# Kernel optimization log

Hardware: AMD Instinct MI355X
Metric: run time of the kernel (lower is better)

Reference implementation:

```python
import jax, jax.numpy as jnp
import numpy as np

N, E = 100000, 400000
IN, HID, H, D = 165, 128, 8, 16  # per-head dim D = HID // H
NUM_CLASSES = 2


def layer_norm(x, g, b, eps=1e-5):
    m = jnp.mean(x, axis=-1, keepdims=True)
    v = jnp.var(x, axis=-1, keepdims=True)
    return (x - m) / jnp.sqrt(v + eps) * g + b


def transformer_conv(x, src, dst, Wq, bq, Wk, bk, Wv, bv, Ws, bs):
    # x: [N, HID]; src/dst: [E]
    n = x.shape[0]
    q = (x @ Wq + bq).reshape(n, H, D)
    k = (x @ Wk + bk).reshape(n, H, D)
    v = (x @ Wv + bv).reshape(n, H, D)
    # per-edge attention logits: [E, H]
    alpha = jnp.sum(q[dst] * k[src], axis=-1) / jnp.sqrt(jnp.float32(D))
    # segment softmax over incoming edges of each destination node
    amax = jax.ops.segment_max(alpha, dst, num_segments=n)          # [N, H]
    amax = jnp.where(jnp.isfinite(amax), amax, 0.0)
    ex = jnp.exp(alpha - amax[dst])                                  # [E, H]
    denom = jax.ops.segment_sum(ex, dst, num_segments=n)            # [N, H]
    a = ex / (denom[dst] + 1e-16)
    msg = v[src] * a[..., None]                                      # [E, H, D]
    out = jax.ops.segment_sum(msg, dst, num_segments=n)             # [N, H, D]
    out = out.reshape(n, H * D)
    # root skip connection (root_weight=True, beta=False in PyG defaults)
    return out + x @ Ws + bs


def setup_inputs() -> dict:
    key = jax.random.key(0)
    ks = jax.random.split(key, 24)
    rn = lambda k, s: (jax.random.normal(k, s, jnp.float32) * 0.05)
    inp = {
        "x": jax.random.normal(ks[0], (N, IN), jnp.float32),
        "edge_index": jax.random.randint(ks[1], (2, E), 0, N, jnp.int32),
        "W_in": rn(ks[2], (IN, HID)), "b_in": jnp.zeros((HID,), jnp.float32),
        # layer 1 TransformerConv
        "Wq1": rn(ks[3], (HID, HID)), "bq1": jnp.zeros((HID,), jnp.float32),
        "Wk1": rn(ks[4], (HID, HID)), "bk1": jnp.zeros((HID,), jnp.float32),
        "Wv1": rn(ks[5], (HID, HID)), "bv1": jnp.zeros((HID,), jnp.float32),
        "Ws1": rn(ks[6], (HID, HID)), "bs1": jnp.zeros((HID,), jnp.float32),
        "g1": jnp.ones((HID,), jnp.float32), "be1": jnp.zeros((HID,), jnp.float32),
        # layer 2 TransformerConv
        "Wq2": rn(ks[7], (HID, HID)), "bq2": jnp.zeros((HID,), jnp.float32),
        "Wk2": rn(ks[8], (HID, HID)), "bk2": jnp.zeros((HID,), jnp.float32),
        "Wv2": rn(ks[9], (HID, HID)), "bv2": jnp.zeros((HID,), jnp.float32),
        "Ws2": rn(ks[10], (HID, HID)), "bs2": jnp.zeros((HID,), jnp.float32),
        "g2": jnp.ones((HID,), jnp.float32), "be2": jnp.zeros((HID,), jnp.float32),
        # classifier MLP
        "Wc1": rn(ks[11], (HID, HID // 2)), "bc1": jnp.zeros((HID // 2,), jnp.float32),
        "Wc2": rn(ks[12], (HID // 2, NUM_CLASSES)), "bc2": jnp.zeros((NUM_CLASSES,), jnp.float32),
    }
    return inp


def reference(x, edge_index, W_in, b_in,
              Wq1, bq1, Wk1, bk1, Wv1, bv1, Ws1, bs1, g1, be1,
              Wq2, bq2, Wk2, bk2, Wv2, bv2, Ws2, bs2, g2, be2,
              Wc1, bc1, Wc2, bc2):
    src, dst = edge_index[0], edge_index[1]
    h = x @ W_in + b_in                                   # input projection
    h_new = transformer_conv(h, src, dst, Wq1, bq1, Wk1, bk1, Wv1, bv1, Ws1, bs1)
    h = layer_norm(h + h_new, g1, be1)                    # dropout = identity (eval)
    h_new = transformer_conv(h, src, dst, Wq2, bq2, Wk2, bk2, Wv2, bv2, Ws2, bs2)
    h = layer_norm(h + h_new, g2, be2)
    return jax.nn.relu(h @ Wc1 + bc1) @ Wc2 + bc2         # [N, num_classes]
```

## Files before the change

kernel.cpp:

```cpp
#include <hip/hip_runtime.h>
#include <hip/hip_bf16.h>

#define NN 100000
#define EE 400000
#define IN_DIM 165
#define KPAD 192
#define HID 128
#define C1 64
#define NC 2
#define SCANB 256
#define NBLK 391
#define NBD2 782

typedef const float* fpp;
typedef __hip_bfloat16 bf16;
typedef __attribute__((ext_vector_type(8))) short s16x8;
typedef __attribute__((ext_vector_type(4))) float f32x4;

__device__ __forceinline__ float bflo(unsigned u) { return __uint_as_float(u << 16); }
__device__ __forceinline__ float bfhi(unsigned u) { return __uint_as_float(u & 0xFFFF0000u); }
__device__ __forceinline__ unsigned short bfbits(float f) {
    bf16 h = __float2bfloat16(f);
    return *reinterpret_cast<unsigned short*>(&h);
}

__global__ void k_cvt_weights(fpp W_in, fpp Wq1, fpp Wk1, fpp Wv1, fpp Ws1,
                              fpp Wq2, fpp Wk2, fpp Wv2, fpp Ws2, fpp Wc1,
                              unsigned short* __restrict__ winpack,
                              unsigned short* __restrict__ wpack,
                              unsigned short* __restrict__ wc1t) {
    int idx = blockIdx.x * blockDim.x + threadIdx.x;
    if (idx < 24576) {
        int n = idx / KPAD, k = idx % KPAD;
        float v = (k < IN_DIM) ? W_in[k * HID + n] : 0.f;
        winpack[idx] = bfbits(v);
    } else if (idx < 155648) {
        int local = idx - 24576;
        int j = local >> 14;
        int l14 = local & 16383;
        int n = l14 >> 7, k = l14 & 127;
        const float* src;
        switch (j) {
            case 0: src = Wq1; break; case 1: src = Wk1; break;
            case 2: src = Wv1; break; case 3: src = Ws1; break;
            case 4: src = Wq2; break; case 5: src = Wk2; break;
            case 6: src = Wv2; break; default: src = Ws2; break;
        }
        wpack[local] = bfbits(src[k * HID + n]);
    } else {
        int local = idx - 155648;
        int n = local >> 7, k = local & 127;
        wc1t[local] = bfbits(Wc1[k * C1 + n]);
    }
}

__global__ void k_cvt_x(fpp x, unsigned short* __restrict__ xb) {
    int i = blockIdx.x * blockDim.x + threadIdx.x;
    int row = i / 24, c = i % 24;
    s16x8 us;
#pragma unroll
    for (int j = 0; j < 8; j++) {
        int col = c * 8 + j;
        float v = (col < IN_DIM) ? x[(size_t)row * IN_DIM + col] : 0.f;
        us[j] = (short)bfbits(v);
    }
    *(s16x8*)(xb + (size_t)row * KPAD + c * 8) = us;
}

__global__ void k_hist(const int* __restrict__ dst, int* __restrict__ deg) {
    int e = blockIdx.x * blockDim.x + threadIdx.x;
    if (e < EE) atomicAdd(&deg[dst[e]], 1);
}
__global__ void k_scan1(const int* __restrict__ deg, int* __restrict__ pos,
                        int* __restrict__ bsum, int n) {
    __shared__ int tmp[SCANB];
    int t = threadIdx.x, i = blockIdx.x * SCANB + t;
    int v = (i < n) ? deg[i] : 0;
    tmp[t] = v; __syncthreads();
    for (int off = 1; off < SCANB; off <<= 1) {
        int x = (t >= off) ? tmp[t - off] : 0;
        __syncthreads();
        tmp[t] += x;
        __syncthreads();
    }
    if (i < n) pos[i] = tmp[t] - v;
    if (t == SCANB - 1) bsum[blockIdx.x] = tmp[t];
}
__global__ void k_scan2(int* __restrict__ bsum, int nb) {
    __shared__ int tmp[512];
    int t = threadIdx.x;
    int v = (t < nb) ? bsum[t] : 0;
    tmp[t] = v; __syncthreads();
    for (int off = 1; off < 512; off <<= 1) {
        int x = (t >= off) ? tmp[t - off] : 0;
        __syncthreads();
        tmp[t] += x;
        __syncthreads();
    }
    if (t < nb) bsum[t] = tmp[t] - v;
}
__global__ void k_scan3(int* __restrict__ pos, const int* __restrict__ bsum, int n) {
    int i = blockIdx.x * blockDim.x + threadIdx.x;
    if (i < n) pos[i] += bsum[blockIdx.x];
}
__global__ void k_fill(const int* __restrict__ src, const int* __restrict__ dst,
                       int* __restrict__ pos, int* __restrict__ esrc) {
    int e = blockIdx.x * blockDim.x + threadIdx.x;
    if (e < EE) {
        int p = atomicAdd(&pos[dst[e]], 1);
        esrc[p] = src[e];
    }
}
__global__ void k_pack_csr(const int* __restrict__ pos, const int* __restrict__ deg,
                           int2* __restrict__ csr2) {
    int i = blockIdx.x * blockDim.x + threadIdx.x;
    if (i < NN) {
        int c = deg[i];
        csr2[i] = make_int2(pos[i] - c, c);
    }
}

__global__ __launch_bounds__(256) void k_dense_in(const unsigned short* __restrict__ xb,
                                                  const unsigned short* __restrict__ winpack,
                                                  fpp b_in, unsigned short* __restrict__ hb) {
    __shared__ unsigned short smem[18432];
    unsigned short* As = smem;
    unsigned short* Ws = smem + 9216;
    int row0 = blockIdx.x * 128;
    int t = threadIdx.x, lane = t & 63, w = t >> 6;
    int quad = lane >> 4, l16 = lane & 15;
    int m_off = (w >> 1) * 64, n_off = (w & 1) * 64;

    f32x4 acc[4][4];
    float bias_v[4];
#pragma unroll
    for (int ni = 0; ni < 4; ni++) bias_v[ni] = b_in[n_off + ni * 16 + l16];
#pragma unroll
    for (int mi = 0; mi < 4; mi++)
#pragma unroll
        for (int ni = 0; ni < 4; ni++)
            acc[mi][ni] = (f32x4){bias_v[ni], bias_v[ni], bias_v[ni], bias_v[ni]};

    for (int kc = 0; kc < 3; kc++) {
        __syncthreads();
        for (int i = 0; i < 4; i++) {
            int g = t + i * 256;
            int r = g >> 3, c = g & 7;
            int rg = min(row0 + r, NN - 1);
            *(s16x8*)(As + r * 72 + c * 8) =
                *(const s16x8*)(xb + (size_t)rg * KPAD + kc * 64 + c * 8);
            *(s16x8*)(Ws + r * 72 + c * 8) =
                *(const s16x8*)(winpack + r * KPAD + kc * 64 + c * 8);
        }
        __syncthreads();
#pragma unroll
        for (int ks = 0; ks < 2; ks++) {
            int k0 = ks * 32;
            s16x8 a[4], b[4];
#pragma unroll
            for (int mi = 0; mi < 4; mi++)
                a[mi] = *(const s16x8*)(As + (m_off + mi * 16 + l16) * 72 + k0 + quad * 8);
#pragma unroll
            for (int ni = 0; ni < 4; ni++)
                b[ni] = *(const s16x8*)(Ws + (n_off + ni * 16 + l16) * 72 + k0 + quad * 8);
#pragma unroll
            for (int mi = 0; mi < 4; mi++)
#pragma unroll
                for (int ni = 0; ni < 4; ni++)
                    acc[mi][ni] = __builtin_amdgcn_mfma_f32_16x16x32_bf16(
                        a[mi], b[ni], acc[mi][ni], 0, 0, 0);
        }
    }
    __syncthreads();
    unsigned short* Cs = smem;
#pragma unroll
    for (int mi = 0; mi < 4; mi++)
#pragma unroll
        for (int ni = 0; ni < 4; ni++)
#pragma unroll
            for (int r = 0; r < 4; r++)
                Cs[(m_off + mi * 16 + quad * 4 + r) * 136 + n_off + ni * 16 + l16] =
                    bfbits(acc[mi][ni][r]);
    __syncthreads();
    for (int i = 0; i < 8; i++) {
        int g = t + i * 256;
        int r = g >> 4, c = g & 15;
        if (row0 + r < NN)
            *(s16x8*)(hb + (size_t)(row0 + r) * HID + c * 8) =
                *(const s16x8*)(Cs + r * 136 + c * 8);
    }
}

__global__ __launch_bounds__(256) void k_dense4(const unsigned short* __restrict__ hb,
                                                const unsigned short* __restrict__ wpackL,
                                                fpp bq, fpp bk, fpp bv, fpp bs,
                                                bf16* __restrict__ qb, bf16* __restrict__ kb,
                                                bf16* __restrict__ vb, bf16* __restrict__ agg) {
    __shared__ unsigned short As[128 * 136];
    __shared__ unsigned short Ws[128 * 136];
    int row0 = blockIdx.x * 128;
    int t = threadIdx.x, lane = t & 63, w = t >> 6;
    int quad = lane >> 4, l16 = lane & 15;
    int m_off = (w >> 1) * 64, n_off = (w & 1) * 64;

    for (int i = 0; i < 8; i++) {
        int g = t + i * 256;
        int r = g >> 4, c = g & 15;
        int rg = min(row0 + r, NN - 1);
        *(s16x8*)(As + r * 136 + c * 8) = *(const s16x8*)(hb + (size_t)rg * HID + c * 8);
    }
    __syncthreads();

    s16x8 afr[4][4];
#pragma unroll
    for (int ks = 0; ks < 4; ks++)
#pragma unroll
        for (int mi = 0; mi < 4; mi++)
            afr[ks][mi] = *(const s16x8*)(As + (m_off + mi * 16 + l16) * 136 + ks * 32 + quad * 8);

    for (int nc = 0; nc < 4; nc++) {
        const float* bp; bf16* tp;
        if (nc == 0)      { bp = bq; tp = qb; }
        else if (nc == 1) { bp = bk; tp = kb; }
        else if (nc == 2) { bp = bv; tp = vb; }
        else              { bp = bs; tp = agg; }

        __syncthreads();
        for (int i = 0; i < 8; i++) {
            int g = t + i * 256;
            int r = g >> 4, c = g & 15;
            *(s16x8*)(Ws + r * 136 + c * 8) =
                *(const s16x8*)(wpackL + nc * 16384 + r * HID + c * 8);
        }
        __syncthreads();

        f32x4 acc[4][4];
        float bias_v[4];
#pragma unroll
        for (int ni = 0; ni < 4; ni++) bias_v[ni] = bp[n_off + ni * 16 + l16];
#pragma unroll
        for (int mi = 0; mi < 4; mi++)
#pragma unroll
            for (int ni = 0; ni < 4; ni++)
                acc[mi][ni] = (f32x4){bias_v[ni], bias_v[ni], bias_v[ni], bias_v[ni]};

#pragma unroll
        for (int ks = 0; ks < 4; ks++) {
            s16x8 b[4];
#pragma unroll
            for (int ni = 0; ni < 4; ni++)
                b[ni] = *(const s16x8*)(Ws + (n_off + ni * 16 + l16) * 136 + ks * 32 + quad * 8);
#pragma unroll
            for (int mi = 0; mi < 4; mi++)
#pragma unroll
                for (int ni = 0; ni < 4; ni++)
                    acc[mi][ni] = __builtin_amdgcn_mfma_f32_16x16x32_bf16(
                        afr[ks][mi], b[ni], acc[mi][ni], 0, 0, 0);
        }
        __syncthreads();

        unsigned short* Cs = Ws;
#pragma unroll
        for (int mi = 0; mi < 4; mi++)
#pragma unroll
            for (int ni = 0; ni < 4; ni++)
#pragma unroll
                for (int r = 0; r < 4; r++)
                    Cs[(m_off + mi * 16 + quad * 4 + r) * 136 + n_off + ni * 16 + l16] =
                        bfbits(acc[mi][ni][r]);
        __syncthreads();
        for (int i = 0; i < 8; i++) {
            int g = t + i * 256;
            int r = g >> 4, c = g & 15;
            if (row0 + r < NN)
                *(s16x8*)((unsigned short*)tp + (size_t)(row0 + r) * HID + c * 8) =
                    *(const s16x8*)(Cs + r * 136 + c * 8);
        }
    }
}

__global__ void k_agg_ln(const bf16* __restrict__ qb, const bf16* __restrict__ kb,
                         const bf16* __restrict__ vb, const int2* __restrict__ csr2,
                         const int* __restrict__ esrc, const bf16* __restrict__ agg,
                         unsigned short* __restrict__ hb, fpp g, fpp b) {
    int wid = (blockIdx.x * blockDim.x + threadIdx.x) >> 6;
    if (wid >= NN) return;
    int lane = threadIdx.x & 63;
    int d = wid;
    unsigned qu = ((const unsigned*)(qb + (size_t)d * HID))[lane];
    float q0 = bflo(qu) * 0.25f, q1 = bfhi(qu) * 0.25f;
    int2 se = csr2[d];
    int start = se.x, cnt = se.y;
    float m = -INFINITY, L = 0.f, o0 = 0.f, o1 = 0.f;
    for (int base = 0; base < cnt; base += 64) {
        int nc = min(64, cnt - base);
        int sj = (lane < nc) ? esrc[start + base + lane] : 0;
        int j = 0;
        for (; j + 1 < nc; j += 2) {
            int s0 = __shfl(sj, j, 64);
            int s1 = __shfl(sj, j + 1, 64);
            unsigned ku0 = ((const unsigned*)(kb + (size_t)s0 * HID))[lane];
            unsigned ku1 = ((const unsigned*)(kb + (size_t)s1 * HID))[lane];
            unsigned vu0 = ((const unsigned*)(vb + (size_t)s0 * HID))[lane];
            unsigned vu1 = ((const unsigned*)(vb + (size_t)s1 * HID))[lane];
            float t0 = q0 * bflo(ku0) + q1 * bfhi(ku0);
            float t1 = q0 * bflo(ku1) + q1 * bfhi(ku1);
            t0 += __shfl_xor(t0, 1, 64); t1 += __shfl_xor(t1, 1, 64);
            t0 += __shfl_xor(t0, 2, 64); t1 += __shfl_xor(t1, 2, 64);
            t0 += __shfl_xor(t0, 4, 64); t1 += __shfl_xor(t1, 4, 64);
            float nm = fmaxf(m, fmaxf(t0, t1));
            float corr = __expf(m - nm);
            float p0 = __expf(t0 - nm), p1 = __expf(t1 - nm);
            L = L * corr + p0 + p1;
            o0 = o0 * corr + p0 * bflo(vu0) + p1 * bflo(vu1);
            o1 = o1 * corr + p0 * bfhi(vu0) + p1 * bfhi(vu1);
            m = nm;
        }
        if (j < nc) {
            int s0 = __shfl(sj, j, 64);
            unsigned ku0 = ((const unsigned*)(kb + (size_t)s0 * HID))[lane];
            unsigned vu0 = ((const unsigned*)(vb + (size_t)s0 * HID))[lane];
            float t0 = q0 * bflo(ku0) + q1 * bfhi(ku0);
            t0 += __shfl_xor(t0, 1, 64);
            t0 += __shfl_xor(t0, 2, 64);
            t0 += __shfl_xor(t0, 4, 64);
            float nm = fmaxf(m, t0);
            float corr = __expf(m - nm);
            float p0 = __expf(t0 - nm);
            L = L * corr + p0;
            o0 = o0 * corr + p0 * bflo(vu0);
            o1 = o1 * corr + p0 * bfhi(vu0);
            m = nm;
        }
    }
    float inv = 1.f / (L + 1e-16f);
    unsigned au = ((const unsigned*)(agg + (size_t)d * HID))[lane];
    unsigned hu = ((const unsigned*)(hb + (size_t)d * HID))[lane];
    float v0 = bflo(hu) + bflo(au) + o0 * inv;
    float v1 = bfhi(hu) + bfhi(au) + o1 * inv;
    float s = v0 + v1, s2 = v0 * v0 + v1 * v1;
    for (int off = 32; off; off >>= 1) {
        s += __shfl_xor(s, off, 64);
        s2 += __shfl_xor(s2, off, 64);
    }
    float mn = s * (1.f / HID);
    float var = s2 * (1.f / HID) - mn * mn;
    float invs = rsqrtf(var + 1e-5f);
    float2 gv = ((const float2*)g)[lane];
    float2 bv = ((const float2*)b)[lane];
    float ox = (v0 - mn) * invs * gv.x + bv.x;
    float oy = (v1 - mn) * invs * gv.y + bv.y;
    ((unsigned*)(hb + (size_t)d * HID))[lane] = ((unsigned)bfbits(oy) << 16) | bfbits(ox);
}

__global__ __launch_bounds__(256) void k_classifier(const unsigned short* __restrict__ hb,
                                                    const unsigned short* __restrict__ wc1t,
                                                    fpp bc1, fpp Wc2, fpp bc2,
                                                    float* __restrict__ out) {
    __shared__ unsigned short As[128 * 136];
    __shared__ unsigned short Ws[64 * 136];
    int row0 = blockIdx.x * 128;
    int t = threadIdx.x, lane = t & 63, w = t >> 6;
    int quad = lane >> 4, l16 = lane & 15;
    int m_off = w * 32;

    for (int i = 0; i < 8; i++) {
        int g = t + i * 256;
        int r = g >> 4, c = g & 15;
        int rg = min(row0 + r, NN - 1);
        *(s16x8*)(As + r * 136 + c * 8) = *(const s16x8*)(hb + (size_t)rg * HID + c * 8);
    }
    for (int i = 0; i < 4; i++) {
        int g = t + i * 256;
        int r = g >> 4, c = g & 15;
        *(s16x8*)(Ws + r * 136 + c * 8) = *(const s16x8*)(wc1t + r * HID + c * 8);
    }
    __syncthreads();

    f32x4 acc[2][4];
    float bias_v[4];
#pragma unroll
    for (int ni = 0; ni < 4; ni++) bias_v[ni] = bc1[ni * 16 + l16];
#pragma unroll
    for (int mi = 0; mi < 2; mi++)
#pragma unroll
        for (int ni = 0; ni < 4; ni++)
            acc[mi][ni] = (f32x4){bias_v[ni], bias_v[ni], bias_v[ni], bias_v[ni]};

#pragma unroll
    for (int ks = 0; ks < 4; ks++) {
        s16x8 a[2], b[4];
#pragma unroll
        for (int mi = 0; mi < 2; mi++)
            a[mi] = *(const s16x8*)(As + (m_off + mi * 16 + l16) * 136 + ks * 32 + quad * 8);
#pragma unroll
        for (int ni = 0; ni < 4; ni++)
            b[ni] = *(const s16x8*)(Ws + (ni * 16 + l16) * 136 + ks * 32 + quad * 8);
#pragma unroll
        for (int mi = 0; mi < 2; mi++)
#pragma unroll
            for (int ni = 0; ni < 4; ni++)
                acc[mi][ni] = __builtin_amdgcn_mfma_f32_16x16x32_bf16(
                    a[mi], b[ni], acc[mi][ni], 0, 0, 0);
    }
    __syncthreads();
    float* Cs = (float*)As;
#pragma unroll
    for (int mi = 0; mi < 2; mi++)
#pragma unroll
        for (int ni = 0; ni < 4; ni++)
#pragma unroll
            for (int r = 0; r < 4; r++)
                Cs[(m_off + mi * 16 + quad * 4 + r) * 68 + ni * 16 + l16] =
                    fmaxf(acc[mi][ni][r], 0.f);
    __syncthreads();

    int row = t >> 1, half = t & 1;
    float p0 = 0.f, p1 = 0.f;
    for (int c = half * 32; c < half * 32 + 32; c++) {
        float v = Cs[row * 68 + c];
        p0 += v * Wc2[c * NC + 0];
        p1 += v * Wc2[c * NC + 1];
    }
    p0 += __shfl_xor(p0, 1, 64);
    p1 += __shfl_xor(p1, 1, 64);
    if (half == 0 && row0 + row < NN) {
        out[(size_t)(row0 + row) * NC + 0] = p0 + bc2[0];
        out[(size_t)(row0 + row) * NC + 1] = p1 + bc2[1];
    }
}

extern "C" void kernel_launch(void* const* d_in, const int* in_sizes, int n_in,
                              void* d_out, int out_size, void* d_ws, size_t ws_size,
                              hipStream_t stream) {
    fpp x = (fpp)d_in[0];
    const int* ei = (const int*)d_in[1];
    const int* src = ei;
    const int* dst = ei + EE;
    fpp W_in = (fpp)d_in[2];  fpp b_in = (fpp)d_in[3];
    fpp Wq1 = (fpp)d_in[4];   fpp bq1 = (fpp)d_in[5];
    fpp Wk1 = (fpp)d_in[6];   fpp bk1 = (fpp)d_in[7];
    fpp Wv1 = (fpp)d_in[8];   fpp bv1 = (fpp)d_in[9];
    fpp Ws1 = (fpp)d_in[10];  fpp bs1 = (fpp)d_in[11];
    fpp g1 = (fpp)d_in[12];   fpp be1 = (fpp)d_in[13];
    fpp Wq2 = (fpp)d_in[14];  fpp bq2 = (fpp)d_in[15];
    fpp Wk2 = (fpp)d_in[16];  fpp bk2 = (fpp)d_in[17];
    fpp Wv2 = (fpp)d_in[18];  fpp bv2 = (fpp)d_in[19];
    fpp Ws2 = (fpp)d_in[20];  fpp bs2 = (fpp)d_in[21];
    fpp g2 = (fpp)d_in[22];   fpp be2 = (fpp)d_in[23];
    fpp Wc1 = (fpp)d_in[24];  fpp bc1 = (fpp)d_in[25];
    fpp Wc2 = (fpp)d_in[26];  fpp bc2 = (fpp)d_in[27];
    float* out = (float*)d_out;

    char* p = (char*)d_ws;
    unsigned short* hb = (unsigned short*)p;  p += (size_t)NN * HID * 2;
    bf16* agg = (bf16*)p;            p += (size_t)NN * HID * 2;
    bf16* qb = (bf16*)p;             p += (size_t)NN * HID * 2;
    bf16* kb = (bf16*)p;             p += (size_t)NN * HID * 2;
    bf16* vb = (bf16*)p;             p += (size_t)NN * HID * 2;
    int* deg = (int*)p;              p += (size_t)NN * 4;
    int* pos = (int*)p;              p += (size_t)NN * 4;
    int2* csr2 = (int2*)p;           p += (size_t)NN * 8;
    int* esrc = (int*)p;             p += (size_t)EE * 4;
    int* bsum = (int*)p;             p += 512 * 4;
    unsigned short* winpack = (unsigned short*)p;  p += 24576 * 2;
    unsigned short* wpack = (unsigned short*)p;    p += 131072 * 2;
    unsigned short* wc1t = (unsigned short*)p;     p += 8192 * 2;
    unsigned short* xb = (unsigned short*)qb;

    const int nE = (EE + 255) / 256;
    const int nNn = (NN + 255) / 256;

    k_cvt_weights<<<640, 256, 0, stream>>>(W_in, Wq1, Wk1, Wv1, Ws1,
                                           Wq2, Wk2, Wv2, Ws2, Wc1,
                                           winpack, wpack, wc1t);
    k_cvt_x<<<9375, 256, 0, stream>>>(x, xb);

    hipMemsetAsync(deg, 0, (size_t)NN * 4, stream);
    k_hist<<<nE, 256, 0, stream>>>(dst, deg);
    k_scan1<<<NBLK, SCANB, 0, stream>>>(deg, pos, bsum, NN);
    k_scan2<<<1, 512, 0, stream>>>(bsum, NBLK);
    k_scan3<<<NBLK, SCANB, 0, stream>>>(pos, bsum, NN);
    k_fill<<<nE, 256, 0, stream>>>(src, dst, pos, esrc);
    k_pack_csr<<<nNn, 256, 0, stream>>>(pos, deg, csr2);

    k_dense_in<<<NBD2, 256, 0, stream>>>(xb, winpack, b_in, hb);

    for (int layer = 0; layer < 2; layer++) {
        fpp bq = layer ? bq2 : bq1, bk = layer ? bk2 : bk1;
        fpp bv = layer ? bv2 : bv1, bs = layer ? bs2 : bs1;
        fpp g = layer ? g2 : g1, be = layer ? be2 : be1;
        const unsigned short* wpackL = wpack + (size_t)layer * 65536;

        k_dense4<<<NBD2, 256, 0, stream>>>(hb, wpackL, bq, bk, bv, bs, qb, kb, vb, agg);
        k_agg_ln<<<(NN * 64 + 255) / 256, 256, 0, stream>>>(qb, kb, vb, csr2, esrc,
                                                            agg, hb, g, be);
    }

    k_classifier<<<NBD2, 256, 0, stream>>>(hb, wc1t, bc1, Wc2, bc2, out);
}
```

Measured before the change: 426.5 us.

## Interleave K and V rows and process two nodes per wavefront in aggregation

Repacks the K and V projection weights and biases so that each source node's keys and values sit interleaved in a single 256-element row, which lets each edge fetch both with one 16-byte load per lane. The aggregation kernel now handles two destination nodes per 64-lane wavefront with 32 lanes each, four channels per lane and fewer shuffle reduction steps. It also folds the CSR packing into the final scan kernel, removing one launch. The cost is extra index arithmetic in weight conversion and the risk of getting the permuted head-channel mapping wrong.

```diff
diff --git a/kernel.cpp b/kernel.cpp
--- a/kernel.cpp
+++ b/kernel.cpp
@@ -26,9 +26,12 @@
 
 __global__ void k_cvt_weights(fpp W_in, fpp Wq1, fpp Wk1, fpp Wv1, fpp Ws1,
                               fpp Wq2, fpp Wk2, fpp Wv2, fpp Ws2, fpp Wc1,
+                              fpp bq1, fpp bk1, fpp bv1, fpp bs1,
+                              fpp bq2, fpp bk2, fpp bv2, fpp bs2,
                               unsigned short* __restrict__ winpack,
                               unsigned short* __restrict__ wpack,
-                              unsigned short* __restrict__ wc1t) {
+                              unsigned short* __restrict__ wc1t,
+                              float* __restrict__ bpack) {
     int idx = blockIdx.x * blockDim.x + threadIdx.x;
     if (idx < 24576) {
         int n = idx / KPAD, k = idx % KPAD;
@@ -36,21 +39,40 @@
         winpack[idx] = bfbits(v);
     } else if (idx < 155648) {
         int local = idx - 24576;
-        int j = local >> 14;
-        int l14 = local & 16383;
+        int layer = local >> 16;
+        int rest = local & 65535;
+        int chunk = rest >> 14;
+        int l14 = rest & 16383;
         int n = l14 >> 7, k = l14 & 127;
         const float* src;
-        switch (j) {
-            case 0: src = Wq1; break; case 1: src = Wk1; break;
-            case 2: src = Wv1; break; case 3: src = Ws1; break;
-            case 4: src = Wq2; break; case 5: src = Wk2; break;
-            case 6: src = Wv2; break; default: src = Ws2; break;
-        }
-        wpack[local] = bfbits(src[k * HID + n]);
-    } else {
+        int col;
+        if (chunk == 0) { src = layer ? Wq2 : Wq1; col = n; }
+        else if (chunk == 3) { src = layer ? Ws2 : Ws1; col = n; }
+        else {
+            int a = ((chunk == 2) ? 16 : 0) + (n >> 3), e = n & 7;
+            src = (e < 4) ? (layer ? Wk2 : Wk1) : (layer ? Wv2 : Wv1);
+            col = 4 * a + (e & 3);
+        }
+        wpack[local] = bfbits(src[k * HID + col]);
+    } else if (idx < 163840) {
         int local = idx - 155648;
         int n = local >> 7, k = local & 127;
         wc1t[local] = bfbits(Wc1[k * C1 + n]);
+    } else if (idx < 164864) {
+        int local = idx - 163840;
+        int layer = local >> 9;
+        int rest = local & 511;
+        int chunk = rest >> 7, n = rest & 127;
+        const float* src;
+        int col;
+        if (chunk == 0) { src = layer ? bq2 : bq1; col = n; }
+        else if (chunk == 3) { src = layer ? bs2 : bs1; col = n; }
+        else {
+            int a = ((chunk == 2) ? 16 : 0) + (n >> 3), e = n & 7;
+            src = (e < 4) ? (layer ? bk2 : bk1) : (layer ? bv2 : bv1);
+            col = 4 * a + (e & 3);
+        }
+        bpack[local] = src[col];
     }
 }
 
@@ -99,9 +121,14 @@
     }
     if (t < nb) bsum[t] = tmp[t] - v;
 }
-__global__ void k_scan3(int* __restrict__ pos, const int* __restrict__ bsum, int n) {
+__global__ void k_scan3(int* __restrict__ pos, const int* __restrict__ bsum,
+                        const int* __restrict__ deg, int2* __restrict__ csr2, int n) {
     int i = blockIdx.x * blockDim.x + threadIdx.x;
-    if (i < n) pos[i] += bsum[blockIdx.x];
+    if (i < n) {
+        int s = pos[i] + bsum[blockIdx.x];
+        pos[i] = s;
+        csr2[i] = make_int2(s, deg[i]);
+    }
 }
 __global__ void k_fill(const int* __restrict__ src, const int* __restrict__ dst,
                        int* __restrict__ pos, int* __restrict__ esrc) {
@@ -109,14 +136,6 @@
     if (e < EE) {
         int p = atomicAdd(&pos[dst[e]], 1);
         esrc[p] = src[e];
-    }
-}
-__global__ void k_pack_csr(const int* __restrict__ pos, const int* __restrict__ deg,
-                           int2* __restrict__ csr2) {
-    int i = blockIdx.x * blockDim.x + threadIdx.x;
-    if (i < NN) {
-        int c = deg[i];
-        csr2[i] = make_int2(pos[i] - c, c);
     }
 }
 
@@ -193,9 +212,9 @@
 
 __global__ __launch_bounds__(256) void k_dense4(const unsigned short* __restrict__ hb,
                                                 const unsigned short* __restrict__ wpackL,
-                                                fpp bq, fpp bk, fpp bv, fpp bs,
-                                                bf16* __restrict__ qb, bf16* __restrict__ kb,
-                                                bf16* __restrict__ vb, bf16* __restrict__ agg) {
+                                                const float* __restrict__ bpackL,
+                                                bf16* __restrict__ qb, bf16* __restrict__ kvb,
+                                                bf16* __restrict__ agg) {
     __shared__ unsigned short As[128 * 136];
     __shared__ unsigned short Ws[128 * 136];
     int row0 = blockIdx.x * 128;
@@ -219,11 +238,12 @@
             afr[ks][mi] = *(const s16x8*)(As + (m_off + mi * 16 + l16) * 136 + ks * 32 + quad * 8);
 
     for (int nc = 0; nc < 4; nc++) {
-        const float* bp; bf16* tp;
-        if (nc == 0)      { bp = bq; tp = qb; }
-        else if (nc == 1) { bp = bk; tp = kb; }
-        else if (nc == 2) { bp = bv; tp = vb; }
-        else              { bp = bs; tp = agg; }
+        unsigned short* tp; int stride;
+        if (nc == 0)      { tp = (unsigned short*)qb;        stride = 128; }
+        else if (nc == 1) { tp = (unsigned short*)kvb;       stride = 256; }
+        else if (nc == 2) { tp = (unsigned short*)kvb + 128; stride = 256; }
+        else              { tp = (unsigned short*)agg;       stride = 128; }
+        const float* bp = bpackL + nc * 128;
 
         __syncthreads();
         for (int i = 0; i < 8; i++) {
@@ -273,84 +293,93 @@
             int g = t + i * 256;
             int r = g >> 4, c = g & 15;
             if (row0 + r < NN)
-                *(s16x8*)((unsigned short*)tp + (size_t)(row0 + r) * HID + c * 8) =
+                *(s16x8*)(tp + (size_t)(row0 + r) * stride + c * 8) =
                     *(const s16x8*)(Cs + r * 136 + c * 8);
         }
     }
 }
 
-__global__ void k_agg_ln(const bf16* __restrict__ qb, const bf16* __restrict__ kb,
-                         const bf16* __restrict__ vb, const int2* __restrict__ csr2,
-                         const int* __restrict__ esrc, const bf16* __restrict__ agg,
-                         unsigned short* __restrict__ hb, fpp g, fpp b) {
-    int wid = (blockIdx.x * blockDim.x + threadIdx.x) >> 6;
-    if (wid >= NN) return;
+__global__ void k_agg_ln(const bf16* __restrict__ qb, const bf16* __restrict__ kvb,
+                         const int2* __restrict__ csr2, const int* __restrict__ esrc,
+                         const bf16* __restrict__ agg, unsigned short* __restrict__ hb,
+                         fpp g, fpp b) {
+    int wv = (blockIdx.x * blockDim.x + threadIdx.x) >> 6;
     int lane = threadIdx.x & 63;
-    int d = wid;
-    unsigned qu = ((const unsigned*)(qb + (size_t)d * HID))[lane];
-    float q0 = bflo(qu) * 0.25f, q1 = bfhi(qu) * 0.25f;
+    int l32 = lane & 31;
+    int d = wv * 2 + (lane >> 5);
+    if (d >= NN) return;
+    uint2 qu = ((const uint2*)(qb + (size_t)d * HID))[l32];
+    float q0 = bflo(qu.x) * 0.25f, q1 = bfhi(qu.x) * 0.25f;
+    float q2 = bflo(qu.y) * 0.25f, q3 = bfhi(qu.y) * 0.25f;
     int2 se = csr2[d];
+    uint2 au = ((const uint2*)(agg + (size_t)d * HID))[l32];
+    uint2 hu = ((const uint2*)(hb + (size_t)d * HID))[l32];
+    float4 gv = ((const float4*)g)[l32];
+    float4 bv = ((const float4*)b)[l32];
     int start = se.x, cnt = se.y;
-    float m = -INFINITY, L = 0.f, o0 = 0.f, o1 = 0.f;
-    for (int base = 0; base < cnt; base += 64) {
-        int nc = min(64, cnt - base);
-        int sj = (lane < nc) ? esrc[start + base + lane] : 0;
+    float m = -INFINITY, L = 0.f, o0 = 0.f, o1 = 0.f, o2 = 0.f, o3 = 0.f;
+    for (int base = 0; base < cnt; base += 32) {
+        int nc = min(32, cnt - base);
+        int sj = (l32 < nc) ? esrc[start + base + l32] : 0;
         int j = 0;
         for (; j + 1 < nc; j += 2) {
-            int s0 = __shfl(sj, j, 64);
-            int s1 = __shfl(sj, j + 1, 64);
-            unsigned ku0 = ((const unsigned*)(kb + (size_t)s0 * HID))[lane];
-            unsigned ku1 = ((const unsigned*)(kb + (size_t)s1 * HID))[lane];
-            unsigned vu0 = ((const unsigned*)(vb + (size_t)s0 * HID))[lane];
-            unsigned vu1 = ((const unsigned*)(vb + (size_t)s1 * HID))[lane];
-            float t0 = q0 * bflo(ku0) + q1 * bfhi(ku0);
-            float t1 = q0 * bflo(ku1) + q1 * bfhi(ku1);
-            t0 += __shfl_xor(t0, 1, 64); t1 += __shfl_xor(t1, 1, 64);
-            t0 += __shfl_xor(t0, 2, 64); t1 += __shfl_xor(t1, 2, 64);
-            t0 += __shfl_xor(t0, 4, 64); t1 += __shfl_xor(t1, 4, 64);
+            int s0 = __shfl(sj, j, 32);
+            int s1 = __shfl(sj, j + 1, 32);
+            uint4 kv0 = ((const uint4*)(kvb + (size_t)s0 * 256))[l32];
+            uint4 kv1 = ((const uint4*)(kvb + (size_t)s1 * 256))[l32];
+            float t0 = q0 * bflo(kv0.x) + q1 * bfhi(kv0.x) + q2 * bflo(kv0.y) + q3 * bfhi(kv0.y);
+            float t1 = q0 * bflo(kv1.x) + q1 * bfhi(kv1.x) + q2 * bflo(kv1.y) + q3 * bfhi(kv1.y);
+            t0 += __shfl_xor(t0, 1); t1 += __shfl_xor(t1, 1);
+            t0 += __shfl_xor(t0, 2); t1 += __shfl_xor(t1, 2);
             float nm = fmaxf(m, fmaxf(t0, t1));
             float corr = __expf(m - nm);
             float p0 = __expf(t0 - nm), p1 = __expf(t1 - nm);
             L = L * corr + p0 + p1;
-            o0 = o0 * corr + p0 * bflo(vu0) + p1 * bflo(vu1);
-            o1 = o1 * corr + p0 * bfhi(vu0) + p1 * bfhi(vu1);
+            o0 = o0 * corr + p0 * bflo(kv0.z) + p1 * bflo(kv1.z);
+            o1 = o1 * corr + p0 * bfhi(kv0.z) + p1 * bfhi(kv1.z);
+            o2 = o2 * corr + p0 * bflo(kv0.w) + p1 * bflo(kv1.w);
+            o3 = o3 * corr + p0 * bfhi(kv0.w) + p1 * bfhi(kv1.w);
             m = nm;
         }
         if (j < nc) {
-            int s0 = __shfl(sj, j, 64);
-            unsigned ku0 = ((const unsigned*)(kb + (size_t)s0 * HID))[lane];
-            unsigned vu0 = ((const unsigned*)(vb + (size_t)s0 * HID))[lane];
-            float t0 = q0 * bflo(ku0) + q1 * bfhi(ku0);
-            t0 += __shfl_xor(t0, 1, 64);
-            t0 += __shfl_xor(t0, 2, 64);
-            t0 += __shfl_xor(t0, 4, 64);
+            int s0 = __shfl(sj, j, 32);
+            uint4 kv0 = ((const uint4*)(kvb + (size_t)s0 * 256))[l32];
+            float t0 = q0 * bflo(kv0.x) + q1 * bfhi(kv0.x) + q2 * bflo(kv0.y) + q3 * bfhi(kv0.y);
+            t0 += __shfl_xor(t0, 1);
+            t0 += __shfl_xor(t0, 2);
             float nm = fmaxf(m, t0);
             float corr = __expf(m - nm);
             float p0 = __expf(t0 - nm);
             L = L * corr + p0;
-            o0 = o0 * corr + p0 * bflo(vu0);
-            o1 = o1 * corr + p0 * bfhi(vu0);
+            o0 = o0 * corr + p0 * bflo(kv0.z);
+            o1 = o1 * corr + p0 * bfhi(kv0.z);
+            o2 = o2 * corr + p0 * bflo(kv0.w);
+            o3 = o3 * corr + p0 * bfhi(kv0.w);
             m = nm;
         }
     }
     float inv = 1.f / (L + 1e-16f);
-    unsigned au = ((const unsigned*)(agg + (size_t)d * HID))[lane];
-    unsigned hu = ((const unsigned*)(hb + (size_t)d * HID))[lane];
-    float v0 = bflo(hu) + bflo(au) + o0 * inv;
-    float v1 = bfhi(hu) + bfhi(au) + o1 * inv;
-    float s = v0 + v1, s2 = v0 * v0 + v1 * v1;
-    for (int off = 32; off; off >>= 1) {
-        s += __shfl_xor(s, off, 64);
-        s2 += __shfl_xor(s2, off, 64);
+    float v0 = bflo(hu.x) + bflo(au.x) + o0 * inv;
+    float v1 = bfhi(hu.x) + bfhi(au.x) + o1 * inv;
+    float v2 = bflo(hu.y) + bflo(au.y) + o2 * inv;
+    float v3 = bfhi(hu.y) + bfhi(au.y) + o3 * inv;
+    float s = v0 + v1 + v2 + v3;
+    float s2 = v0 * v0 + v1 * v1 + v2 * v2 + v3 * v3;
+    for (int off = 16; off; off >>= 1) {
+        s += __shfl_xor(s, off);
+        s2 += __shfl_xor(s2, off);
     }
     float mn = s * (1.f / HID);
     float var = s2 * (1.f / HID) - mn * mn;
     float invs = rsqrtf(var + 1e-5f);
-    float2 gv = ((const float2*)g)[lane];
-    float2 bv = ((const float2*)b)[lane];
     float ox = (v0 - mn) * invs * gv.x + bv.x;
     float oy = (v1 - mn) * invs * gv.y + bv.y;
-    ((unsigned*)(hb + (size_t)d * HID))[lane] = ((unsigned)bfbits(oy) << 16) | bfbits(ox);
+    float oz = (v2 - mn) * invs * gv.z + bv.z;
+    float ow = (v3 - mn) * invs * gv.w + bv.w;
+    uint2 outw;
+    outw.x = ((unsigned)bfbits(oy) << 16) | bfbits(ox);
+    outw.y = ((unsigned)bfbits(ow) << 16) | bfbits(oz);
+    ((uint2*)(hb + (size_t)d * HID))[l32] = outw;
 }
 
 __global__ __launch_bounds__(256) void k_classifier(const unsigned short* __restrict__ hb,
@@ -456,8 +485,7 @@
     unsigned short* hb = (unsigned short*)p;  p += (size_t)NN * HID * 2;
     bf16* agg = (bf16*)p;            p += (size_t)NN * HID * 2;
     bf16* qb = (bf16*)p;             p += (size_t)NN * HID * 2;
-    bf16* kb = (bf16*)p;             p += (size_t)NN * HID * 2;
-    bf16* vb = (bf16*)p;             p += (size_t)NN * HID * 2;
+    bf16* kvb = (bf16*)p;            p += (size_t)NN * 256 * 2;
     int* deg = (int*)p;              p += (size_t)NN * 4;
     int* pos = (int*)p;              p += (size_t)NN * 4;
     int2* csr2 = (int2*)p;           p += (size_t)NN * 8;
@@ -466,35 +494,34 @@
     unsigned short* winpack = (unsigned short*)p;  p += 24576 * 2;
     unsigned short* wpack = (unsigned short*)p;    p += 131072 * 2;
     unsigned short* wc1t = (unsigned short*)p;     p += 8192 * 2;
+    float* bpack = (float*)p;                      p += 1024 * 4;
     unsigned short* xb = (unsigned short*)qb;
 
     const int nE = (EE + 255) / 256;
     const int nNn = (NN + 255) / 256;
 
-    k_cvt_weights<<<640, 256, 0, stream>>>(W_in, Wq1, Wk1, Wv1, Ws1,
+    k_cvt_weights<<<644, 256, 0, stream>>>(W_in, Wq1, Wk1, Wv1, Ws1,
                                            Wq2, Wk2, Wv2, Ws2, Wc1,
-                                           winpack, wpack, wc1t);
+                                           bq1, bk1, bv1, bs1, bq2, bk2, bv2, bs2,
+                                           winpack, wpack, wc1t, bpack);
     k_cvt_x<<<9375, 256, 0, stream>>>(x, xb);
 
     hipMemsetAsync(deg, 0, (size_t)NN * 4, stream);
     k_hist<<<nE, 256, 0, stream>>>(dst, deg);
     k_scan1<<<NBLK, SCANB, 0, stream>>>(deg, pos, bsum, NN);
     k_scan2<<<1, 512, 0, stream>>>(bsum, NBLK);
-    k_scan3<<<NBLK, SCANB, 0, stream>>>(pos, bsum, NN);
+    k_scan3<<<NBLK, SCANB, 0, stream>>>(pos, bsum, deg, csr2, NN);
     k_fill<<<nE, 256, 0, stream>>>(src, dst, pos, esrc);
-    k_pack_csr<<<nNn, 256, 0, stream>>>(pos, deg, csr2);
 
     k_dense_in<<<NBD2, 256, 0, stream>>>(xb, winpack, b_in, hb);
 
     for (int layer = 0; layer < 2; layer++) {
-        fpp bq = layer ? bq2 : bq1, bk = layer ? bk2 : bk1;
-        fpp bv = layer ? bv2 : bv1, bs = layer ? bs2 : bs1;
         fpp g = layer ? g2 : g1, be = layer ? be2 : be1;
         const unsigned short* wpackL = wpack + (size_t)layer * 65536;
-
-        k_dense4<<<NBD2, 256, 0, stream>>>(hb, wpackL, bq, bk, bv, bs, qb, kb, vb, agg);
-        k_agg_ln<<<(NN * 64 + 255) / 256, 256, 0, stream>>>(qb, kb, vb, csr2, esrc,
-                                                            agg, hb, g, be);
+        const float* bpackL = bpack + (size_t)layer * 512;
+
+        k_dense4<<<NBD2, 256, 0, stream>>>(hb, wpackL, bpackL, qb, kvb, agg);
+        k_agg_ln<<<12500, 256, 0, stream>>>(qb, kvb, csr2, esrc, agg, hb, g, be);
     }
 
     k_classifier<<<NBD2, 256, 0, stream>>>(hb, wc1t, bc1, Wc2, bc2, out);
```

Measured after the change: 404.1 us. 5.3% less time.
